# Performance work log

Measured on AMD Instinct MI355X. Metric: run time of the kernel, lower is better.

Reference implementation:

```python
import jax, jax.numpy as jnp
import numpy as np

D_MODEL = 512


def setup_inputs() -> dict:
    key = jax.random.key(0)
    ks = jax.random.split(key, 9)
    B, S, D = 2, 4096, D_MODEL
    scale = 1.0 / np.sqrt(D)
    return {
        "Q": jax.random.normal(ks[0], (B, S, D), dtype=jnp.float32),
        "K": jax.random.normal(ks[1], (B, S, D), dtype=jnp.float32),
        "V": jax.random.normal(ks[2], (B, S, D), dtype=jnp.float32),
        "W_q": jax.random.normal(ks[3], (D, D), dtype=jnp.float32) * scale,
        "b_q": jax.random.normal(ks[4], (D,), dtype=jnp.float32) * scale,
        "W_k": jax.random.normal(ks[5], (D, D), dtype=jnp.float32) * scale,
        "b_k": jax.random.normal(ks[6], (D,), dtype=jnp.float32) * scale,
        "W_v": jax.random.normal(ks[7], (D, D), dtype=jnp.float32) * scale,
        "b_v": jax.random.normal(ks[8], (D,), dtype=jnp.float32) * scale,
    }


def reference(Q, K, V, W_q, b_q, W_k, b_k, W_v, b_v):
    # Linear projections (torch Linear: x @ W.T + b)
    q = jnp.einsum("bsd,ed->bse", Q, W_q) + b_q  # [B,S,D]
    k = jnp.einsum("bsd,ed->bse", K, W_k) + b_k
    v = jnp.einsum("bsd,ed->bse", V, W_v) + b_v
    d_k = k.shape[-1]
    scores = jnp.einsum("bqd,bkd->bqk", q, k) / jnp.sqrt(jnp.asarray(d_k, q.dtype))
    attn = jax.nn.softmax(scores, axis=-1)  # [B,S,S]
    return jnp.einsum("bqk,bkd->bqd", attn, v)
```

## Files before the change

### kernel.cpp

```cpp
#include <hip/hip_runtime.h>
#include <hip/hip_bf16.h>
#include <math.h>
#include <stdint.h>

typedef __attribute__((ext_vector_type(8))) short short8;
typedef __attribute__((ext_vector_type(4))) float floatx4;
typedef __attribute__((ext_vector_type(4))) unsigned short ushort4v;

__device__ __forceinline__ void gload_lds16(const void* g, void* lds) {
    __builtin_amdgcn_global_load_lds(
        (__attribute__((address_space(1))) void*)(g),
        (__attribute__((address_space(3))) void*)(lds), 16, 0, 0);
}
__device__ __forceinline__ float bf16bits_to_f(unsigned short u) {
    union { unsigned int i; float f; } x; x.i = ((unsigned int)u) << 16; return x.f;
}
__device__ __forceinline__ unsigned short f_to_bf16bits(float f) {
    union { float f; unsigned int i; } x; x.f = f;
    unsigned int lsb = (x.i >> 16) & 1u;
    x.i += 0x7fffu + lsb;
    return (unsigned short)(x.i >> 16);
}

__global__ __launch_bounds__(256) void conv_all_kernel(
    const float* __restrict__ Q, const float* __restrict__ K, const float* __restrict__ V,
    const float* __restrict__ Wq, const float* __restrict__ Wk, const float* __restrict__ Wv,
    const float* __restrict__ bq, const float* __restrict__ bk, const float* __restrict__ bv,
    unsigned short* __restrict__ qkv,
    unsigned short* __restrict__ Wo,
    unsigned short* __restrict__ bo)
{
    const int gid = blockIdx.x;
    const float* src; unsigned short* dst; int idx;
    if (gid < 12288) {
        const int seg = gid >> 12, blk = gid & 4095;
        src = (seg == 0) ? Q : (seg == 1) ? K : V;
        dst = qkv + (size_t)seg * 4194304;
        idx = (blk * 256 + threadIdx.x) * 4;
    } else if (gid < 13056) {
        const int t = gid - 12288, m = t >> 8, blk = t & 255;
        src = (m == 0) ? Wq : (m == 1) ? Wk : Wv;
        dst = Wo + (size_t)m * 262144;
        idx = (blk * 256 + threadIdx.x) * 4;
    } else {
        const int m = gid - 13056;
        if (threadIdx.x >= 128) return;
        src = (m == 0) ? bq : (m == 1) ? bk : bv;
        dst = bo + (size_t)m * 512;
        idx = threadIdx.x * 4;
    }
    float4 v = *(const float4*)&src[idx];
    ushort4v o;
    o[0] = f_to_bf16bits(v.x); o[1] = f_to_bf16bits(v.y);
    o[2] = f_to_bf16bits(v.z); o[3] = f_to_bf16bits(v.w);
    *(ushort4v*)&dst[idx] = o;
}

__global__ __launch_bounds__(256) void conv1_kernel(
    const float* __restrict__ in, unsigned short* __restrict__ out)
{
    const int idx = (blockIdx.x * 256 + threadIdx.x) * 4;
    float4 v = *(const float4*)&in[idx];
    ushort4v o;
    o[0] = f_to_bf16bits(v.x); o[1] = f_to_bf16bits(v.y);
    o[2] = f_to_bf16bits(v.z); o[3] = f_to_bf16bits(v.w);
    *(ushort4v*)&out[idx] = o;
}

__global__ __launch_bounds__(256) void conv_wb_kernel(
    const float* __restrict__ Wq, const float* __restrict__ Wk, const float* __restrict__ Wv,
    const float* __restrict__ bq, const float* __restrict__ bk, const float* __restrict__ bv,
    unsigned short* __restrict__ Wo, unsigned short* __restrict__ bo)
{
    const int m = blockIdx.y;
    const float* W = (m == 0) ? Wq : (m == 1) ? Wk : Wv;
    const float* b = (m == 0) ? bq : (m == 1) ? bk : bv;
    if (blockIdx.x < 256) {
        const int idx = (blockIdx.x * 256 + threadIdx.x) * 4;
        float4 v = *(const float4*)&W[idx];
        ushort4v o;
        o[0] = f_to_bf16bits(v.x); o[1] = f_to_bf16bits(v.y);
        o[2] = f_to_bf16bits(v.z); o[3] = f_to_bf16bits(v.w);
        *(ushort4v*)&Wo[(size_t)m * 262144 + idx] = o;
    } else if (threadIdx.x < 128) {
        const int idx = threadIdx.x * 4;
        float4 v = *(const float4*)&b[idx];
        ushort4v o;
        o[0] = f_to_bf16bits(v.x); o[1] = f_to_bf16bits(v.y);
        o[2] = f_to_bf16bits(v.z); o[3] = f_to_bf16bits(v.w);
        *(ushort4v*)&bo[(size_t)m * 512 + idx] = o;
    }
}

__global__ __launch_bounds__(256, 2) void proj_kernel(
    const unsigned short* __restrict__ Xall,
    size_t xstride, int mode_base,
    const unsigned short* __restrict__ Wall,
    const unsigned short* __restrict__ ball,
    unsigned short* __restrict__ qbuf,
    unsigned short* __restrict__ kbuf,
    unsigned short* __restrict__ vTbuf,
    float qscale)
{
    __shared__ __align__(16) unsigned short Xs[128 * 64];
    __shared__ __align__(16) unsigned short Ws[128 * 64];

    const int mode = mode_base + blockIdx.y;
    const unsigned short* X = Xall + (size_t)blockIdx.y * xstride;
    const unsigned short* W = Wall + (size_t)mode * 262144;
    const unsigned short* bias = ball + (size_t)mode * 512;

    const int tid = threadIdx.x;
    const int wave = tid >> 6, lane = tid & 63, quad = lane >> 4, l15 = lane & 15;
    const int m0 = (int)(blockIdx.x >> 2) << 7;
    const int n0 = (int)(blockIdx.x & 3) << 7;
    const int mw = (wave >> 1) << 6, nw = (wave & 1) << 6;

    floatx4 acc[4][4];
    #pragma unroll
    for (int i = 0; i < 4; i++)
        #pragma unroll
        for (int j = 0; j < 4; j++) acc[i][j] = floatx4{0.f, 0.f, 0.f, 0.f};

    for (int kt = 0; kt < 512; kt += 64) {
        #pragma unroll
        for (int i = 0; i < 4; i++) {
            const int r0 = wave * 32 + i * 8;
            gload_lds16(X + (size_t)(m0 + r0 + (lane >> 3)) * 512 + kt + (lane & 7) * 8, &Xs[r0 * 64]);
            gload_lds16(W + (size_t)(n0 + r0 + (lane >> 3)) * 512 + kt + (lane & 7) * 8, &Ws[r0 * 64]);
        }
        __syncthreads();
        #pragma unroll
        for (int kk = 0; kk < 64; kk += 32) {
            short8 a[4], b[4];
            #pragma unroll
            for (int i = 0; i < 4; i++) a[i] = *(const short8*)&Xs[(mw + 16 * i + l15) * 64 + kk + quad * 8];
            #pragma unroll
            for (int j = 0; j < 4; j++) b[j] = *(const short8*)&Ws[(nw + 16 * j + l15) * 64 + kk + quad * 8];
            #pragma unroll
            for (int i = 0; i < 4; i++)
                #pragma unroll
                for (int j = 0; j < 4; j++)
                    acc[i][j] = __builtin_amdgcn_mfma_f32_16x16x32_bf16(a[i], b[j], acc[i][j], 0, 0, 0);
        }
        __syncthreads();
    }

    float bfj[4];
    #pragma unroll
    for (int j = 0; j < 4; j++) bfj[j] = bf16bits_to_f(bias[n0 + nw + 16 * j + l15]);

    if (mode < 2) {
        unsigned short* out = (mode == 0) ? qbuf : kbuf;
        const float s = (mode == 0) ? qscale : 1.0f;
        #pragma unroll
        for (int i = 0; i < 4; i++) {
            const int mrow = m0 + mw + 16 * i + quad * 4;
            #pragma unroll
            for (int j = 0; j < 4; j++) {
                const int n = n0 + nw + 16 * j + l15;
                #pragma unroll
                for (int r = 0; r < 4; r++)
                    out[(size_t)(mrow + r) * 512 + n] = f_to_bf16bits((acc[i][j][r] + bfj[j]) * s);
            }
        }
    } else {
        #pragma unroll
        for (int i = 0; i < 4; i++) {
            const int mrow = m0 + mw + 16 * i + quad * 4;
            const int bb = mrow >> 12;
            const int k4 = mrow & 4095;
            const size_t kpart = (size_t)bb * 2097152 + (size_t)(k4 >> 3) * 128 + (k4 & 7);
            #pragma unroll
            for (int j = 0; j < 4; j++) {
                const int n = n0 + nw + 16 * j + l15;
                ushort4v pk;
                #pragma unroll
                for (int r = 0; r < 4; r++) pk[r] = f_to_bf16bits(acc[i][j][r] + bfj[j]);
                *(ushort4v*)&vTbuf[kpart + (size_t)(n >> 4) * 65536 + (n & 15) * 8] = pk;
            }
        }
    }
}

template <int NSPLIT>
__global__ __launch_bounds__(256, 2) void attn_kernel(
    const unsigned short* __restrict__ q,
    const unsigned short* __restrict__ k,
    const unsigned short* __restrict__ vT,
    unsigned short* __restrict__ num,
    float* __restrict__ denom)
{
    constexpr int TK  = 32;
    constexpr int KST = 520;
    constexpr int PST = 40;
    __shared__ __align__(16) unsigned short Ks[TK * KST];
    __shared__ __align__(16) unsigned short Ps[64 * PST];

    const int tid = threadIdx.x;
    const int wave = tid >> 6, lane = tid & 63, quad = lane >> 4, l15 = lane & 15;
    const int bid = blockIdx.x;
    const int sp   = bid & (NSPLIT - 1);
    const int qblk = bid / NSPLIT;
    const int bb = qblk >> 6;
    const int q0 = (qblk & 63) << 6;
    const size_t rowbase = (size_t)bb * 4096 + q0;

    short8 qf[16];
    {
        const unsigned short* qrow = q + (rowbase + 16 * wave + l15) * 512;
        #pragma unroll
        for (int t = 0; t < 16; t++) qf[t] = *(const short8*)&qrow[t * 32 + quad * 8];
    }

    floatx4 oacc[4][8];
    #pragma unroll
    for (int i = 0; i < 4; i++)
        #pragma unroll
        for (int c = 0; c < 8; c++) oacc[i][c] = floatx4{0.f, 0.f, 0.f, 0.f};
    float dsum[4] = {0.f, 0.f, 0.f, 0.f};

    const unsigned short* kb = k + (size_t)bb * 4096 * 512;
    const unsigned short* vbase = vT + (size_t)bb * 2097152
                                + (size_t)(8 * wave) * 65536 + quad * 128 + l15 * 8;

    const int jbeg = sp * (4096 / NSPLIT);
    const int jend = jbeg + (4096 / NSPLIT);
    for (int j0 = jbeg; j0 < jend; j0 += TK) {
        #pragma unroll
        for (int r = 0; r < 8; r++) {
            const int row = wave * 8 + r;
            gload_lds16(kb + (size_t)(j0 + row) * 512 + lane * 8, &Ks[row * KST]);
        }
        __syncthreads();

        short8 vf[8];
        #pragma unroll
        for (int c = 0; c < 8; c++)
            vf[c] = *(const short8*)&vbase[(size_t)c * 65536 + (j0 << 4)];

        floatx4 sA[2], sB[2];
        sA[0] = sA[1] = sB[0] = sB[1] = floatx4{0.f, 0.f, 0.f, 0.f};
        #pragma unroll
        for (int t = 0; t < 16; t += 2) {
            #pragma unroll
            for (int c = 0; c < 2; c++) {
                short8 b0 = *(const short8*)&Ks[(c * 16 + l15) * KST + t * 32 + quad * 8];
                sA[c] = __builtin_amdgcn_mfma_f32_16x16x32_bf16(qf[t], b0, sA[c], 0, 0, 0);
                short8 b1 = *(const short8*)&Ks[(c * 16 + l15) * KST + (t + 1) * 32 + quad * 8];
                sB[c] = __builtin_amdgcn_mfma_f32_16x16x32_bf16(qf[t + 1], b1, sB[c], 0, 0, 0);
            }
        }
        #pragma unroll
        for (int c = 0; c < 2; c++) {
            #pragma unroll
            for (int r = 0; r < 4; r++) {
                const float p = __expf(fminf(sA[c][r] + sB[c][r], 30.0f));
                const unsigned short pb = f_to_bf16bits(p);
                dsum[r] += bf16bits_to_f(pb);
                Ps[(16 * wave + quad * 4 + r) * PST + c * 16 + l15] = pb;
            }
        }
        __syncthreads();

        short8 ap[4];
        #pragma unroll
        for (int i = 0; i < 4; i++) ap[i] = *(const short8*)&Ps[(16 * i + l15) * PST + quad * 8];
        #pragma unroll
        for (int c = 0; c < 8; c++) {
            #pragma unroll
            for (int i = 0; i < 4; i++)
                oacc[i][c] = __builtin_amdgcn_mfma_f32_16x16x32_bf16(ap[i], vf[c], oacc[i][c], 0, 0, 0);
        }
    }

    #pragma unroll
    for (int r = 0; r < 4; r++) {
        float v = dsum[r];
        v += __shfl_xor(v, 1);
        v += __shfl_xor(v, 2);
        v += __shfl_xor(v, 4);
        v += __shfl_xor(v, 8);
        dsum[r] = v;
    }
    if (l15 == 0) {
        #pragma unroll
        for (int r = 0; r < 4; r++)
            denom[(size_t)sp * 8192 + rowbase + 16 * wave + quad * 4 + r] = dsum[r];
    }

    #pragma unroll
    for (int i = 0; i < 4; i++) {
        #pragma unroll
        for (int r = 0; r < 4; r++) {
            const size_t row = rowbase + 16 * i + quad * 4 + r;
            short8 pk;
            #pragma unroll
            for (int c = 0; c < 8; c++) pk[c] = (short)f_to_bf16bits(oacc[i][c][r]);
            *(short8*)&num[((size_t)sp * 8192 + row) * 512 + wave * 128 + l15 * 8] = pk;
        }
    }
}

__global__ __launch_bounds__(256) void combine_kernel(
    const unsigned short* __restrict__ num,
    const float* __restrict__ denom,
    float* __restrict__ out,
    int nsplit)
{
    const int gid = blockIdx.x * 256 + threadIdx.x;
    const int srow = gid >> 6;
    const int sub = gid & 63;
    const int w = sub >> 4, l15 = sub & 15;
    float s[8];
    #pragma unroll
    for (int e = 0; e < 8; e++) s[e] = 0.f;
    float den = 0.f;
    for (int sp = 0; sp < nsplit; sp++) {
        den += denom[(size_t)sp * 8192 + srow];
        short8 v = *(const short8*)(num + ((size_t)sp * 8192 + srow) * 512 + w * 128 + l15 * 8);
        #pragma unroll
        for (int e = 0; e < 8; e++) s[e] += bf16bits_to_f((unsigned short)v[e]);
    }
    const float inv = 1.0f / den;
    float* op = out + (size_t)srow * 512 + w * 128 + l15;
    #pragma unroll
    for (int c = 0; c < 8; c++) op[16 * c] = s[c] * inv;
}

extern "C" void kernel_launch(void* const* d_in, const int* in_sizes, int n_in,
                              void* d_out, int out_size, void* d_ws, size_t ws_size,
                              hipStream_t stream)
{
    (void)in_sizes; (void)n_in; (void)out_size;
    const float* Qin = (const float*)d_in[0];
    const float* Kin = (const float*)d_in[1];
    const float* Vin = (const float*)d_in[2];
    const float* Wq  = (const float*)d_in[3];
    const float* bq  = (const float*)d_in[4];
    const float* Wk  = (const float*)d_in[5];
    const float* bk  = (const float*)d_in[6];
    const float* Wv  = (const float*)d_in[7];
    const float* bv  = (const float*)d_in[8];

    const size_t M   = (size_t)8192 * 512;
    const size_t WS_ = (size_t)512 * 512;

    auto need = [&](size_t sa, int ns) -> size_t {
        return (sa + 3 * M) * 2 + 3 * WS_ * 2 + 3 * 512 * 2 + 64 + (size_t)ns * 8192 * 4;
    };
    int nsplit; size_t sa; bool batched;
    if      (ws_size >= need(4 * M, 4)) { nsplit = 4; sa = 4 * M; batched = true; }
    else if (ws_size >= need(3 * M, 2)) { nsplit = 2; sa = 3 * M; batched = true; }
    else                                { nsplit = 1; sa = 1 * M; batched = false; }

    unsigned short* ws    = (unsigned short*)d_ws;
    unsigned short* slotA = ws;
    unsigned short* qs    = ws + sa;
    unsigned short* ks    = qs + M;
    unsigned short* vT    = ks + M;
    unsigned short* Wc    = vT + M;
    unsigned short* bc    = Wc + 3 * WS_;
    float* denom = (float*)(((uintptr_t)(bc + 3 * 512) + 15) & ~(uintptr_t)15);
    unsigned short* numb = slotA;

    const float qscale = 1.0f / sqrtf(512.0f);

    if (batched) {
        conv_all_kernel<<<dim3(13059), dim3(256), 0, stream>>>(
            Qin, Kin, Vin, Wq, Wk, Wv, bq, bk, bv, slotA, Wc, bc);
        proj_kernel<<<dim3(256, 3), dim3(256), 0, stream>>>(
            slotA, M, 0, Wc, bc, qs, ks, vT, qscale);
    } else {
        conv_wb_kernel<<<dim3(257, 3), dim3(256), 0, stream>>>(Wq, Wk, Wv, bq, bk, bv, Wc, bc);
        const float* Xin[3] = { Qin, Kin, Vin };
        for (int m = 0; m < 3; m++) {
            conv1_kernel<<<dim3(4096), dim3(256), 0, stream>>>(Xin[m], slotA);
            proj_kernel<<<dim3(256, 1), dim3(256), 0, stream>>>(
                slotA, 0, m, Wc, bc, qs, ks, vT, qscale);
        }
    }

    if (nsplit == 4)
        attn_kernel<4><<<dim3(512), dim3(256), 0, stream>>>(qs, ks, vT, numb, denom);
    else if (nsplit == 2)
        attn_kernel<2><<<dim3(256), dim3(256), 0, stream>>>(qs, ks, vT, numb, denom);
    else
        attn_kernel<1><<<dim3(128), dim3(256), 0, stream>>>(qs, ks, vT, numb, denom);

    combine_kernel<<<dim3(2048), dim3(256), 0, stream>>>(
        numb, denom, (float*)d_out, nsplit);
}
```

Measured before the change: 224.9 us.

## Double-buffer K tile in LDS with async prefetch of next tile

The attention kernel now keeps two LDS buffers for the K tile. The global-to-LDS load of the next tile is issued right after the barrier, so it overlaps the current QK MFMAs, softmax and PV compute. The two __syncthreads are replaced by custom barriers that wait only on vmcnt or only on lgkmcnt. The cost is roughly double the LDS footprint per block, which could limit occupancy, and the hand-written waitcnt encodings must be correct.

```diff
diff --git a/kernel.cpp b/kernel.cpp
--- a/kernel.cpp
+++ b/kernel.cpp
@@ -20,6 +20,14 @@
     unsigned int lsb = (x.i >> 16) & 1u;
     x.i += 0x7fffu + lsb;
     return (unsigned short)(x.i >> 16);
+}
+__device__ __forceinline__ void barrier_vm0() {
+    __builtin_amdgcn_s_waitcnt(0x0F70);
+    __builtin_amdgcn_s_barrier();
+}
+__device__ __forceinline__ void barrier_lgkm0() {
+    __builtin_amdgcn_s_waitcnt(0xC07F);
+    __builtin_amdgcn_s_barrier();
 }
 
 __global__ __launch_bounds__(256) void conv_all_kernel(
@@ -194,7 +202,7 @@
     constexpr int TK  = 32;
     constexpr int KST = 520;
     constexpr int PST = 40;
-    __shared__ __align__(16) unsigned short Ks[TK * KST];
+    __shared__ __align__(16) unsigned short Ks[2][TK * KST];
     __shared__ __align__(16) unsigned short Ps[64 * PST];
 
     const int tid = threadIdx.x;
@@ -225,29 +233,43 @@
                                 + (size_t)(8 * wave) * 65536 + quad * 128 + l15 * 8;
 
     const int jbeg = sp * (4096 / NSPLIT);
-    const int jend = jbeg + (4096 / NSPLIT);
-    for (int j0 = jbeg; j0 < jend; j0 += TK) {
-        #pragma unroll
-        for (int r = 0; r < 8; r++) {
-            const int row = wave * 8 + r;
-            gload_lds16(kb + (size_t)(j0 + row) * 512 + lane * 8, &Ks[row * KST]);
-        }
-        __syncthreads();
+    constexpr int NITER = (4096 / NSPLIT) / TK;
+
+    #pragma unroll
+    for (int r = 0; r < 8; r++) {
+        const int row = wave * 8 + r;
+        gload_lds16(kb + (size_t)(jbeg + row) * 512 + lane * 8, &Ks[0][row * KST]);
+    }
+
+    for (int it = 0; it < NITER; ++it) {
+        const int j0 = jbeg + it * TK;
+        const int buf = it & 1;
+
+        barrier_vm0();
 
         short8 vf[8];
         #pragma unroll
         for (int c = 0; c < 8; c++)
             vf[c] = *(const short8*)&vbase[(size_t)c * 65536 + (j0 << 4)];
 
+        if (it + 1 < NITER) {
+            #pragma unroll
+            for (int r = 0; r < 8; r++) {
+                const int row = wave * 8 + r;
+                gload_lds16(kb + (size_t)(j0 + TK + row) * 512 + lane * 8,
+                            &Ks[buf ^ 1][row * KST]);
+            }
+        }
+
         floatx4 sA[2], sB[2];
         sA[0] = sA[1] = sB[0] = sB[1] = floatx4{0.f, 0.f, 0.f, 0.f};
         #pragma unroll
         for (int t = 0; t < 16; t += 2) {
             #pragma unroll
             for (int c = 0; c < 2; c++) {
-                short8 b0 = *(const short8*)&Ks[(c * 16 + l15) * KST + t * 32 + quad * 8];
+                short8 b0 = *(const short8*)&Ks[buf][(c * 16 + l15) * KST + t * 32 + quad * 8];
                 sA[c] = __builtin_amdgcn_mfma_f32_16x16x32_bf16(qf[t], b0, sA[c], 0, 0, 0);
-                short8 b1 = *(const short8*)&Ks[(c * 16 + l15) * KST + (t + 1) * 32 + quad * 8];
+                short8 b1 = *(const short8*)&Ks[buf][(c * 16 + l15) * KST + (t + 1) * 32 + quad * 8];
                 sB[c] = __builtin_amdgcn_mfma_f32_16x16x32_bf16(qf[t + 1], b1, sB[c], 0, 0, 0);
             }
         }
@@ -261,7 +283,7 @@
                 Ps[(16 * wave + quad * 4 + r) * PST + c * 16 + l15] = pb;
             }
         }
-        __syncthreads();
+        barrier_lgkm0();
 
         short8 ap[4];
         #pragma unroll
```

After: 225.2 us. No clear change (+0.2%).

## Split QK^T reduction dim across wave pairs to halve K LDS reads

Applied to the files above, without the earlier changes.

In the QK^T phase, each wave now handles 32 query rows over half of the 512-wide head dimension instead of 16 rows over the full width. Each K fragment loaded from LDS is then reused for two MFMAs, halving K shared-memory reads per wave. Partial scores are swapped between paired waves through a new shared exchange buffer, which costs an extra __syncthreads per tile. Each wave computes exp for half the columns, so the denominator buffer doubles and the combine kernel sums twice as many partials.

```diff
diff --git a/kernel.cpp b/kernel.cpp
--- a/kernel.cpp
+++ b/kernel.cpp
@@ -196,9 +196,11 @@
     constexpr int PST = 40;
     __shared__ __align__(16) unsigned short Ks[TK * KST];
     __shared__ __align__(16) unsigned short Ps[64 * PST];
+    __shared__ __align__(16) float Xch[2][2][2][64][4];
 
     const int tid = threadIdx.x;
     const int wave = tid >> 6, lane = tid & 63, quad = lane >> 4, l15 = lane & 15;
+    const int mgrp = wave >> 1, dh = wave & 1;
     const int bid = blockIdx.x;
     const int sp   = bid & (NSPLIT - 1);
     const int qblk = bid / NSPLIT;
@@ -208,9 +210,12 @@
 
     short8 qf[16];
     {
-        const unsigned short* qrow = q + (rowbase + 16 * wave + l15) * 512;
-        #pragma unroll
-        for (int t = 0; t < 16; t++) qf[t] = *(const short8*)&qrow[t * 32 + quad * 8];
+        const unsigned short* qbase = q + (rowbase + 32 * mgrp + l15) * 512 + dh * 256;
+        #pragma unroll
+        for (int i2 = 0; i2 < 2; i2++)
+            #pragma unroll
+            for (int t = 0; t < 8; t++)
+                qf[i2 * 8 + t] = *(const short8*)&qbase[i2 * 16 * 512 + t * 32 + quad * 8];
     }
 
     floatx4 oacc[4][8];
@@ -218,7 +223,11 @@
     for (int i = 0; i < 4; i++)
         #pragma unroll
         for (int c = 0; c < 8; c++) oacc[i][c] = floatx4{0.f, 0.f, 0.f, 0.f};
-    float dsum[4] = {0.f, 0.f, 0.f, 0.f};
+    float dsum[2][4];
+    #pragma unroll
+    for (int i2 = 0; i2 < 2; i2++)
+        #pragma unroll
+        for (int r = 0; r < 4; r++) dsum[i2][r] = 0.f;
 
     const unsigned short* kb = k + (size_t)bb * 4096 * 512;
     const unsigned short* vbase = vT + (size_t)bb * 2097152
@@ -239,26 +248,36 @@
         for (int c = 0; c < 8; c++)
             vf[c] = *(const short8*)&vbase[(size_t)c * 65536 + (j0 << 4)];
 
-        floatx4 sA[2], sB[2];
-        sA[0] = sA[1] = sB[0] = sB[1] = floatx4{0.f, 0.f, 0.f, 0.f};
-        #pragma unroll
-        for (int t = 0; t < 16; t += 2) {
+        floatx4 sacc[2][2];
+        sacc[0][0] = sacc[0][1] = sacc[1][0] = sacc[1][1] = floatx4{0.f, 0.f, 0.f, 0.f};
+        #pragma unroll
+        for (int t = 0; t < 8; t++) {
             #pragma unroll
             for (int c = 0; c < 2; c++) {
-                short8 b0 = *(const short8*)&Ks[(c * 16 + l15) * KST + t * 32 + quad * 8];
-                sA[c] = __builtin_amdgcn_mfma_f32_16x16x32_bf16(qf[t], b0, sA[c], 0, 0, 0);
-                short8 b1 = *(const short8*)&Ks[(c * 16 + l15) * KST + (t + 1) * 32 + quad * 8];
-                sB[c] = __builtin_amdgcn_mfma_f32_16x16x32_bf16(qf[t + 1], b1, sB[c], 0, 0, 0);
+                short8 b = *(const short8*)&Ks[(c * 16 + l15) * KST + dh * 256 + t * 32 + quad * 8];
+                sacc[0][c] = __builtin_amdgcn_mfma_f32_16x16x32_bf16(qf[t],     b, sacc[0][c], 0, 0, 0);
+                sacc[1][c] = __builtin_amdgcn_mfma_f32_16x16x32_bf16(qf[8 + t], b, sacc[1][c], 0, 0, 0);
             }
         }
-        #pragma unroll
-        for (int c = 0; c < 2; c++) {
+
+        *(floatx4*)&Xch[mgrp][1 - dh][0][lane][0] = sacc[0][1 - dh];
+        *(floatx4*)&Xch[mgrp][1 - dh][1][lane][0] = sacc[1][1 - dh];
+        __syncthreads();
+        {
+            floatx4 p0 = *(const floatx4*)&Xch[mgrp][dh][0][lane][0];
+            floatx4 p1 = *(const floatx4*)&Xch[mgrp][dh][1][lane][0];
+            #pragma unroll
+            for (int r = 0; r < 4; r++) { sacc[0][dh][r] += p0[r]; sacc[1][dh][r] += p1[r]; }
+        }
+
+        #pragma unroll
+        for (int i2 = 0; i2 < 2; i2++) {
             #pragma unroll
             for (int r = 0; r < 4; r++) {
-                const float p = __expf(fminf(sA[c][r] + sB[c][r], 30.0f));
+                const float p = __expf(fminf(sacc[i2][dh][r], 30.0f));
                 const unsigned short pb = f_to_bf16bits(p);
-                dsum[r] += bf16bits_to_f(pb);
-                Ps[(16 * wave + quad * 4 + r) * PST + c * 16 + l15] = pb;
+                dsum[i2][r] += bf16bits_to_f(pb);
+                Ps[(32 * mgrp + 16 * i2 + quad * 4 + r) * PST + dh * 16 + l15] = pb;
             }
         }
         __syncthreads();
@@ -275,18 +294,19 @@
     }
 
     #pragma unroll
-    for (int r = 0; r < 4; r++) {
-        float v = dsum[r];
-        v += __shfl_xor(v, 1);
-        v += __shfl_xor(v, 2);
-        v += __shfl_xor(v, 4);
-        v += __shfl_xor(v, 8);
-        dsum[r] = v;
-    }
-    if (l15 == 0) {
-        #pragma unroll
-        for (int r = 0; r < 4; r++)
-            denom[(size_t)sp * 8192 + rowbase + 16 * wave + quad * 4 + r] = dsum[r];
+    for (int i2 = 0; i2 < 2; i2++) {
+        #pragma unroll
+        for (int r = 0; r < 4; r++) {
+            float v = dsum[i2][r];
+            v += __shfl_xor(v, 1);
+            v += __shfl_xor(v, 2);
+            v += __shfl_xor(v, 4);
+            v += __shfl_xor(v, 8);
+            if (l15 == 0) {
+                const size_t row = rowbase + 32 * mgrp + 16 * i2 + quad * 4 + r;
+                denom[(size_t)(sp * 2 + dh) * 8192 + row] = v;
+            }
+        }
     }
 
     #pragma unroll
@@ -316,8 +336,9 @@
     #pragma unroll
     for (int e = 0; e < 8; e++) s[e] = 0.f;
     float den = 0.f;
+    for (int sp = 0; sp < 2 * nsplit; sp++)
+        den += denom[(size_t)sp * 8192 + srow];
     for (int sp = 0; sp < nsplit; sp++) {
-        den += denom[(size_t)sp * 8192 + srow];
         short8 v = *(const short8*)(num + ((size_t)sp * 8192 + srow) * 512 + w * 128 + l15 * 8);
         #pragma unroll
         for (int e = 0; e < 8; e++) s[e] += bf16bits_to_f((unsigned short)v[e]);
@@ -347,7 +368,7 @@
     const size_t WS_ = (size_t)512 * 512;
 
     auto need = [&](size_t sa, int ns) -> size_t {
-        return (sa + 3 * M) * 2 + 3 * WS_ * 2 + 3 * 512 * 2 + 64 + (size_t)ns * 8192 * 4;
+        return (sa + 3 * M) * 2 + 3 * WS_ * 2 + 3 * 512 * 2 + 64 + (size_t)ns * 2 * 8192 * 4;
     };
     int nsplit; size_t sa; bool batched;
     if      (ws_size >= need(4 * M, 4)) { nsplit = 4; sa = 4 * M; batched = true; }
```

Result: slower. 279.6 us (+24.4%).
